# Performance work log

Hardware: AMD Instinct MI355X
Metric: run time of the kernel (lower is better)

## Reference

```python
import jax, jax.numpy as jnp
import numpy as np


def setup_inputs() -> dict:
    key = jax.random.key(0)
    ks = jax.random.split(key, 6)
    B, T = 512, 32768  # batch of audio segments, samples per segment
    return {
        "x": jax.random.normal(ks[0], (B, T), dtype=jnp.float32),
        "g": jax.random.normal(ks[1], (1,), dtype=jnp.float32),
        "r": jax.random.normal(ks[2], (1,), dtype=jnp.float32),
        "m_hp": jax.random.normal(ks[3], (1,), dtype=jnp.float32),
        "m_bp": jax.random.normal(ks[4], (1,), dtype=jnp.float32),
        "m_lp": jax.random.normal(ks[5], (1,), dtype=jnp.float32),
    }


def _biquad_coeffs(g, r, m_hp, m_bp, m_lp):
    # DSVF parameterization: g = tan(pi*sigmoid(g_raw)/2), r = softplus(r_raw)
    gg = jnp.tan(jnp.pi * jax.nn.sigmoid(g) / 2.0)
    rr = jax.nn.softplus(r)
    g2 = gg * gg
    b0 = g2 * m_lp + gg * m_bp + m_hp
    b1 = 2.0 * g2 * m_lp - 2.0 * m_hp
    b2 = g2 * m_lp - gg * m_bp + m_hp
    a0 = g2 + 2.0 * rr * gg + 1.0
    a1 = 2.0 * g2 - 2.0
    a2 = g2 - 2.0 * rr * gg + 1.0
    # scipy.signal.lfilter normalizes by a[0]
    inv_a0 = 1.0 / jnp.squeeze(a0)
    return (jnp.squeeze(b0) * inv_a0, jnp.squeeze(b1) * inv_a0,
            jnp.squeeze(b2) * inv_a0, jnppy_squeeze(a1) * inv_a0 if False else jnp.squeeze(a1) * inv_a0,
            jnp.squeeze(a2) * inv_a0)


def reference(x, g, r, m_hp, m_bp, m_lp):
    """Biquad IIR (direct form II transposed), zero initial state,
    matching scipy.signal.lfilter(b, a, x) along the last axis of x [B, T]."""
    b0, b1, b2, a1, a2 = _biquad_coeffs(g, r, m_hp, m_bp, m_lp)

    def step(carry, xt):  # xt: [B]
        z1, z2 = carry
        y = b0 * xt + z1
        z1n = b1 * xt - a1 * y + z2
        z2n = b2 * xt - a2 * y
        return (z1n, z2n), y

    B = x.shape[0]
    z0 = (jnp.zeros((B,), x.dtype), jnp.zeros((B,), x.dtype))
    _, y_t = jax.lax.scan(step, z0, x.T)  # scan over time: [T, B]
    return y_t.T  # [B, T]
```

## Files before the change

kernel.cpp:

```cpp
#include <hip/hip_runtime.h>
#include <math.h>


namespace {
constexpr int kB = 512;
constexpr int kT = 32768;
constexpr int kChunk = 64;
constexpr int kNChunk = kT / kChunk;
constexpr int kScanThreads = 256;
constexpr int kStride = kChunk + 1;
}

__device__ inline void coeffs_f32(const float* g, const float* r,
                                  const float* mhp, const float* mbp,
                                  const float* mlp, float& b0, float& b1,
                                  float& b2, float& a1, float& a2) {
  float graw = g[0], rraw = r[0];
  float sig = 1.0f / (1.0f + expf(-graw));
  float gg = tanf(1.5707963267948966f * sig);
  float rr = (rraw > 20.0f) ? rraw : log1pf(expf(rraw));
  float g2 = gg * gg;
  float m_hp = mhp[0], m_bp = mbp[0], m_lp = mlp[0];
  float B0 = g2 * m_lp + gg * m_bp + m_hp;
  float B1 = 2.0f * g2 * m_lp - 2.0f * m_hp;
  float B2 = g2 * m_lp - gg * m_bp + m_hp;
  float A0 = g2 + 2.0f * rr * gg + 1.0f;
  float A1 = 2.0f * g2 - 2.0f;
  float A2 = g2 - 2.0f * rr * gg + 1.0f;
  float inv = 1.0f / A0;
  b0 = B0 * inv; b1 = B1 * inv; b2 = B2 * inv;
  a1 = A1 * inv; a2 = A2 * inv;
}

#define IIR_STEP(xx, yy)                                         \
  do {                                                           \
    yy = fmaf(b0, xx, z1);                                       \
    z1 = fmaf(na1, yy, fmaf(b1, xx, z2));                        \
    z2 = fmaf(na2, yy, b2 * xx);                                 \
  } while (0)

__global__ __launch_bounds__(64) void k_partial(
    const float* __restrict__ x, const float* g, const float* r,
    const float* mhp, const float* mbp, const float* mlp,
    float2* __restrict__ st) {
  __shared__ float buf[64 * kStride];
  int lane = threadIdx.x;

  float b0, b1, b2, a1, a2;
  coeffs_f32(g, r, mhp, mbp, mlp, b0, b1, b2, a1, a2);
  float na1 = -a1, na2 = -a2;

  const float4* xv = (const float4*)x + (size_t)blockIdx.x * 1024;
  float4 v[16];
#pragma unroll
  for (int i = 0; i < 16; ++i) v[i] = xv[i * 64 + lane];

#pragma unroll
  for (int i = 0; i < 16; ++i) {
    int f = i * 64 + lane;
    int base = (f >> 4) * kStride + ((f & 15) << 2);
    buf[base] = v[i].x; buf[base + 1] = v[i].y;
    buf[base + 2] = v[i].z; buf[base + 3] = v[i].w;
  }
  __syncthreads();
#pragma unroll
  for (int i = 0; i < 16; ++i) {
    int base = lane * kStride + (i << 2);
    v[i] = make_float4(buf[base], buf[base + 1], buf[base + 2], buf[base + 3]);
  }

  float z1 = 0.f, z2 = 0.f;
#pragma unroll
  for (int i = 0; i < 16; ++i) {
    float y;
    IIR_STEP(v[i].x, y); IIR_STEP(v[i].y, y);
    IIR_STEP(v[i].z, y); IIR_STEP(v[i].w, y);
  }
  st[(size_t)blockIdx.x * 64 + lane] = make_float2(z1, z2);
}

__global__ __launch_bounds__(kScanThreads) void k_scan(
    float2* __restrict__ st, const float* g, const float* r,
    const float* mhp, const float* mbp, const float* mlp) {
  int row = blockIdx.x;
  int t = threadIdx.x;

  float b0f, b1f, b2f, a1f, a2f;
  coeffs_f32(g, r, mhp, mbp, mlp, b0f, b1f, b2f, a1f, a2f);
  double m00 = -(double)a1f, m01 = 1.0, m10 = -(double)a2f, m11 = 0.0;
  for (int i = 0; i < 6; ++i) {
    double t00 = m00 * m00 + m01 * m10;
    double t01 = m00 * m01 + m01 * m11;
    double t10 = m10 * m00 + m11 * m10;
    double t11 = m10 * m01 + m11 * m11;
    m00 = t00; m01 = t01; m10 = t10; m11 = t11;
  }
  double p00 = m00, p01 = m01, p10 = m10, p11 = m11;

  float2* rowp = st + (size_t)row * kNChunk;
  float4 ld = ((const float4*)rowp)[t];
  double d0x = (double)ld.x, d0y = (double)ld.y;
  double d1x = (double)ld.z, d1y = (double)ld.w;

  double a1v = p00 * d0x + p01 * d0y + d1x;
  double a2v = p10 * d0x + p11 * d0y + d1y;
  double w00 = p00 * p00 + p01 * p10, w01 = p00 * p01 + p01 * p11;
  double w10 = p10 * p00 + p11 * p10, w11 = p10 * p01 + p11 * p11;

  __shared__ double s1[kScanThreads], s2[kScanThreads];
  for (int o = 1; o < kScanThreads; o <<= 1) {
    s1[t] = a1v; s2[t] = a2v;
    __syncthreads();
    double q1 = 0.0, q2 = 0.0;
    if (t >= o) { q1 = s1[t - o]; q2 = s2[t - o]; }
    __syncthreads();
    a1v += w00 * q1 + w01 * q2;
    a2v += w10 * q1 + w11 * q2;
    double t00 = w00 * w00 + w01 * w10, t01 = w00 * w01 + w01 * w11;
    double t10 = w10 * w00 + w11 * w10, t11 = w10 * w01 + w11 * w11;
    w00 = t00; w01 = t01; w10 = t10; w11 = t11;
  }
  s1[t] = a1v; s2[t] = a2v;
  __syncthreads();
  double e1 = 0.0, e2 = 0.0;
  if (t > 0) { e1 = s1[t - 1]; e2 = s2[t - 1]; }
  double i1 = p00 * e1 + p01 * e2 + d0x;
  double i2 = p10 * e1 + p11 * e2 + d0y;
  ((float4*)rowp)[t] = make_float4((float)e1, (float)e2, (float)i1, (float)i2);
}

__global__ __launch_bounds__(64) void k_final(
    const float* __restrict__ x, const float2* __restrict__ st,
    const float* g, const float* r, const float* mhp, const float* mbp,
    const float* mlp, float* __restrict__ out) {
  __shared__ float buf[64 * kStride];
  int lane = threadIdx.x;

  float b0, b1, b2, a1, a2;
  coeffs_f32(g, r, mhp, mbp, mlp, b0, b1, b2, a1, a2);
  float na1 = -a1, na2 = -a2;

  const float4* xv = (const float4*)x + (size_t)blockIdx.x * 1024;
  float4 v[16];
#pragma unroll
  for (int i = 0; i < 16; ++i) v[i] = xv[i * 64 + lane];

#pragma unroll
  for (int i = 0; i < 16; ++i) {
    int f = i * 64 + lane;
    int base = (f >> 4) * kStride + ((f & 15) << 2);
    buf[base] = v[i].x; buf[base + 1] = v[i].y;
    buf[base + 2] = v[i].z; buf[base + 3] = v[i].w;
  }
  __syncthreads();
#pragma unroll
  for (int i = 0; i < 16; ++i) {
    int base = lane * kStride + (i << 2);
    v[i] = make_float4(buf[base], buf[base + 1], buf[base + 2], buf[base + 3]);
  }

  float2 s0 = st[(size_t)blockIdx.x * 64 + lane];
  float z1 = s0.x, z2 = s0.y;
#pragma unroll
  for (int i = 0; i < 16; ++i) {
    float4 o;
    IIR_STEP(v[i].x, o.x); IIR_STEP(v[i].y, o.y);
    IIR_STEP(v[i].z, o.z); IIR_STEP(v[i].w, o.w);
    v[i] = o;
  }

#pragma unroll
  for (int i = 0; i < 16; ++i) {
    int base = lane * kStride + (i << 2);
    buf[base] = v[i].x; buf[base + 1] = v[i].y;
    buf[base + 2] = v[i].z; buf[base + 3] = v[i].w;
  }
  __syncthreads();
  float4* yv = (float4*)out + (size_t)blockIdx.x * 1024;
#pragma unroll
  for (int i = 0; i < 16; ++i) {
    int f = i * 64 + lane;
    int base = (f >> 4) * kStride + ((f & 15) << 2);
    yv[f] = make_float4(buf[base], buf[base + 1], buf[base + 2], buf[base + 3]);
  }
}

extern "C" void kernel_launch(void* const* d_in, const int* in_sizes, int n_in,
                              void* d_out, int out_size, void* d_ws,
                              size_t ws_size, hipStream_t stream) {
  const float* x   = (const float*)d_in[0];
  const float* g   = (const float*)d_in[1];
  const float* r   = (const float*)d_in[2];
  const float* mhp = (const float*)d_in[3];
  const float* mbp = (const float*)d_in[4];
  const float* mlp = (const float*)d_in[5];
  float* out = (float*)d_out;
  float2* st = (float2*)d_ws;

  const int nblocks = kB * kNChunk / 64;
  k_partial<<<nblocks, 64, 0, stream>>>(x, g, r, mhp, mbp, mlp, st);
  k_scan<<<kB, kScanThreads, 0, stream>>>(st, g, r, mhp, mbp, mlp);
  k_final<<<nblocks, 64, 0, stream>>>(x, st, g, r, mhp, mbp, mlp, out);
}
```

Before: 135.2 us.

## Fuse partial, scan and final IIR passes into one row-per-block kernel

Replaces the three-kernel chunked scan (partial state pass, per-row state scan, final pass) with a single kernel where each 512-thread block owns one full row. Each thread filters its 64-sample chunk held in registers, the block does a double-precision matrix-affine prefix scan over chunk states in shared memory, and each thread then reruns its chunk from the corrected state. This removes the second read of x from global memory, the workspace round trip, and two launches. In exchange it uses large blocks with about 133 KB of shared memory each, which limits occupancy, and the 9-step scan with two barriers per step now sits inside the main kernel.

```diff
diff --git a/kernel.cpp b/kernel.cpp
--- a/kernel.cpp
+++ b/kernel.cpp
@@ -3,12 +3,12 @@
 
 
 namespace {
-constexpr int kB = 512;
 constexpr int kT = 32768;
+constexpr int kThreads = 512;
 constexpr int kChunk = 64;
-constexpr int kNChunk = kT / kChunk;
-constexpr int kScanThreads = 256;
 constexpr int kStride = kChunk + 1;
+constexpr int kWaveLds = 64 * kStride;
+constexpr int kSegQuads = 1024;
 }
 
 __device__ inline void coeffs_f32(const float* g, const float* r,
@@ -39,144 +39,95 @@
     z2 = fmaf(na2, yy, b2 * xx);                                 \
   } while (0)
 
-__global__ __launch_bounds__(64) void k_partial(
+#define MAT_SQ(w00, w01, w10, w11)                               \
+  do {                                                           \
+    double t00 = w00 * w00 + w01 * w10;                          \
+    double t01 = w00 * w01 + w01 * w11;                          \
+    double t10 = w10 * w00 + w11 * w10;                          \
+    double t11 = w10 * w01 + w11 * w11;                          \
+    w00 = t00; w01 = t01; w10 = t10; w11 = t11;                  \
+  } while (0)
+
+__global__ __launch_bounds__(kThreads) void k_fused(
     const float* __restrict__ x, const float* g, const float* r,
     const float* mhp, const float* mbp, const float* mlp,
-    float2* __restrict__ st) {
-  __shared__ float buf[64 * kStride];
-  int lane = threadIdx.x;
+    float* __restrict__ out) {
+  __shared__ float xb[8 * kWaveLds];
+  __shared__ double s1[kThreads], s2[kThreads];
+
+  const int t = threadIdx.x;
+  const int lane = t & 63;
+  const int wave = t >> 6;
+  const size_t rowoff = (size_t)blockIdx.x * kT;
 
   float b0, b1, b2, a1, a2;
   coeffs_f32(g, r, mhp, mbp, mlp, b0, b1, b2, a1, a2);
   float na1 = -a1, na2 = -a2;
 
-  const float4* xv = (const float4*)x + (size_t)blockIdx.x * 1024;
-  float4 v[16];
+  const float4* xv = (const float4*)(x + rowoff) + wave * kSegQuads;
+  float* buf = &xb[wave * kWaveLds];
+  float4 c[16];
 #pragma unroll
-  for (int i = 0; i < 16; ++i) v[i] = xv[i * 64 + lane];
-
+  for (int i = 0; i < 16; ++i) c[i] = xv[i * 64 + lane];
 #pragma unroll
   for (int i = 0; i < 16; ++i) {
     int f = i * 64 + lane;
     int base = (f >> 4) * kStride + ((f & 15) << 2);
-    buf[base] = v[i].x; buf[base + 1] = v[i].y;
-    buf[base + 2] = v[i].z; buf[base + 3] = v[i].w;
+    buf[base] = c[i].x; buf[base + 1] = c[i].y;
+    buf[base + 2] = c[i].z; buf[base + 3] = c[i].w;
   }
   __syncthreads();
 #pragma unroll
   for (int i = 0; i < 16; ++i) {
     int base = lane * kStride + (i << 2);
-    v[i] = make_float4(buf[base], buf[base + 1], buf[base + 2], buf[base + 3]);
+    c[i] = make_float4(buf[base], buf[base + 1], buf[base + 2], buf[base + 3]);
   }
 
   float z1 = 0.f, z2 = 0.f;
 #pragma unroll
   for (int i = 0; i < 16; ++i) {
     float y;
-    IIR_STEP(v[i].x, y); IIR_STEP(v[i].y, y);
-    IIR_STEP(v[i].z, y); IIR_STEP(v[i].w, y);
+    IIR_STEP(c[i].x, y); IIR_STEP(c[i].y, y);
+    IIR_STEP(c[i].z, y); IIR_STEP(c[i].w, y);
   }
-  st[(size_t)blockIdx.x * 64 + lane] = make_float2(z1, z2);
-}
 
-__global__ __launch_bounds__(kScanThreads) void k_scan(
-    float2* __restrict__ st, const float* g, const float* r,
-    const float* mhp, const float* mbp, const float* mlp) {
-  int row = blockIdx.x;
-  int t = threadIdx.x;
+  double w00 = -(double)a1, w01 = 1.0, w10 = -(double)a2, w11 = 0.0;
+#pragma unroll
+  for (int i = 0; i < 6; ++i) MAT_SQ(w00, w01, w10, w11);
 
-  float b0f, b1f, b2f, a1f, a2f;
-  coeffs_f32(g, r, mhp, mbp, mlp, b0f, b1f, b2f, a1f, a2f);
-  double m00 = -(double)a1f, m01 = 1.0, m10 = -(double)a2f, m11 = 0.0;
-  for (int i = 0; i < 6; ++i) {
-    double t00 = m00 * m00 + m01 * m10;
-    double t01 = m00 * m01 + m01 * m11;
-    double t10 = m10 * m00 + m11 * m10;
-    double t11 = m10 * m01 + m11 * m11;
-    m00 = t00; m01 = t01; m10 = t10; m11 = t11;
+  double A0 = (double)z1, A1 = (double)z2;
+  for (int o = 1; o < kThreads; o <<= 1) {
+    s1[t] = A0; s2[t] = A1;
+    __syncthreads();
+    double q0 = 0.0, q1 = 0.0;
+    if (t >= o) { q0 = s1[t - o]; q1 = s2[t - o]; }
+    __syncthreads();
+    A0 += w00 * q0 + w01 * q1;
+    A1 += w10 * q0 + w11 * q1;
+    MAT_SQ(w00, w01, w10, w11);
   }
-  double p00 = m00, p01 = m01, p10 = m10, p11 = m11;
+  s1[t] = A0; s2[t] = A1;
+  __syncthreads();
+  double e0 = 0.0, e1 = 0.0;
+  if (t > 0) { e0 = s1[t - 1]; e1 = s2[t - 1]; }
 
-  float2* rowp = st + (size_t)row * kNChunk;
-  float4 ld = ((const float4*)rowp)[t];
-  double d0x = (double)ld.x, d0y = (double)ld.y;
-  double d1x = (double)ld.z, d1y = (double)ld.w;
-
-  double a1v = p00 * d0x + p01 * d0y + d1x;
-  double a2v = p10 * d0x + p11 * d0y + d1y;
-  double w00 = p00 * p00 + p01 * p10, w01 = p00 * p01 + p01 * p11;
-  double w10 = p10 * p00 + p11 * p10, w11 = p10 * p01 + p11 * p11;
-
-  __shared__ double s1[kScanThreads], s2[kScanThreads];
-  for (int o = 1; o < kScanThreads; o <<= 1) {
-    s1[t] = a1v; s2[t] = a2v;
-    __syncthreads();
-    double q1 = 0.0, q2 = 0.0;
-    if (t >= o) { q1 = s1[t - o]; q2 = s2[t - o]; }
-    __syncthreads();
-    a1v += w00 * q1 + w01 * q2;
-    a2v += w10 * q1 + w11 * q2;
-    double t00 = w00 * w00 + w01 * w10, t01 = w00 * w01 + w01 * w11;
-    double t10 = w10 * w00 + w11 * w10, t11 = w10 * w01 + w11 * w11;
-    w00 = t00; w01 = t01; w10 = t10; w11 = t11;
-  }
-  s1[t] = a1v; s2[t] = a2v;
-  __syncthreads();
-  double e1 = 0.0, e2 = 0.0;
-  if (t > 0) { e1 = s1[t - 1]; e2 = s2[t - 1]; }
-  double i1 = p00 * e1 + p01 * e2 + d0x;
-  double i2 = p10 * e1 + p11 * e2 + d0y;
-  ((float4*)rowp)[t] = make_float4((float)e1, (float)e2, (float)i1, (float)i2);
-}
-
-__global__ __launch_bounds__(64) void k_final(
-    const float* __restrict__ x, const float2* __restrict__ st,
-    const float* g, const float* r, const float* mhp, const float* mbp,
-    const float* mlp, float* __restrict__ out) {
-  __shared__ float buf[64 * kStride];
-  int lane = threadIdx.x;
-
-  float b0, b1, b2, a1, a2;
-  coeffs_f32(g, r, mhp, mbp, mlp, b0, b1, b2, a1, a2);
-  float na1 = -a1, na2 = -a2;
-
-  const float4* xv = (const float4*)x + (size_t)blockIdx.x * 1024;
-  float4 v[16];
-#pragma unroll
-  for (int i = 0; i < 16; ++i) v[i] = xv[i * 64 + lane];
-
+  z1 = (float)e0; z2 = (float)e1;
 #pragma unroll
   for (int i = 0; i < 16; ++i) {
-    int f = i * 64 + lane;
-    int base = (f >> 4) * kStride + ((f & 15) << 2);
-    buf[base] = v[i].x; buf[base + 1] = v[i].y;
-    buf[base + 2] = v[i].z; buf[base + 3] = v[i].w;
+    float4 o4;
+    IIR_STEP(c[i].x, o4.x); IIR_STEP(c[i].y, o4.y);
+    IIR_STEP(c[i].z, o4.z); IIR_STEP(c[i].w, o4.w);
+    c[i] = o4;
   }
-  __syncthreads();
 #pragma unroll
   for (int i = 0; i < 16; ++i) {
     int base = lane * kStride + (i << 2);
-    v[i] = make_float4(buf[base], buf[base + 1], buf[base + 2], buf[base + 3]);
-  }
-
-  float2 s0 = st[(size_t)blockIdx.x * 64 + lane];
-  float z1 = s0.x, z2 = s0.y;
-#pragma unroll
-  for (int i = 0; i < 16; ++i) {
-    float4 o;
-    IIR_STEP(v[i].x, o.x); IIR_STEP(v[i].y, o.y);
-    IIR_STEP(v[i].z, o.z); IIR_STEP(v[i].w, o.w);
-    v[i] = o;
-  }
-
-#pragma unroll
-  for (int i = 0; i < 16; ++i) {
-    int base = lane * kStride + (i << 2);
-    buf[base] = v[i].x; buf[base + 1] = v[i].y;
-    buf[base + 2] = v[i].z; buf[base + 3] = v[i].w;
+    buf[base] = c[i].x; buf[base + 1] = c[i].y;
+    buf[base + 2] = c[i].z; buf[base + 3] = c[i].w;
   }
   __syncthreads();
-  float4* yv = (float4*)out + (size_t)blockIdx.x * 1024;
+
+  float4* yv = (float4*)(out + rowoff) + wave * kSegQuads;
 #pragma unroll
   for (int i = 0; i < 16; ++i) {
     int f = i * 64 + lane;
@@ -195,10 +146,7 @@
   const float* mbp = (const float*)d_in[4];
   const float* mlp = (const float*)d_in[5];
   float* out = (float*)d_out;
-  float2* st = (float2*)d_ws;
+  (void)d_ws; (void)ws_size;
 
-  const int nblocks = kB * kNChunk / 64;
-  k_partial<<<nblocks, 64, 0, stream>>>(x, g, r, mhp, mbp, mlp, st);
-  k_scan<<<kB, kScanThreads, 0, stream>>>(st, g, r, mhp, mbp, mlp);
-  k_final<<<nblocks, 64, 0, stream>>>(x, st, g, r, mhp, mbp, mlp, out);
+  k_fused<<<512, kThreads, 0, stream>>>(x, g, r, mhp, mbp, mlp, out);
 }
```

After: 129.9 us. 3.9% less time.
